# Performance work log

Measured on AMD Instinct MI355X. Metric: run time of the kernel, lower is better.

The kernel has to match this reference:

```python
import jax, jax.numpy as jnp
import numpy as np

N, E, D = 10000, 160000, 256
EPS = 1e-5


def layer_norm(x, gamma, beta):
    mu = jnp.mean(x, axis=-1, keepdims=True)
    var = jnp.var(x, axis=-1, keepdims=True)
    return (x - mu) * jax.lax.rsqrt(var + EPS) * gamma + beta


def mlp(x, w1, b1, w2, b2):
    return jax.nn.relu(x @ w1 + b1) @ w2 + b2


def setup_inputs() -> dict:
    key = jax.random.key(0)
    ks = jax.random.split(key, 16)
    s = lambda fan_in: 1.0 / np.sqrt(fan_in)
    inp = {
        'x': jax.random.normal(ks[0], (N, D), jnp.float32),
        'edge_index': jax.random.randint(ks[1], (2, E), 0, N, jnp.int64),
        'edge_attr': jax.random.normal(ks[2], (E, D), jnp.float32),
        # edge MLP: in 3D=768 -> hidden 2D=512 -> out D=256, then LN
        'e_w1': jax.random.uniform(ks[3], (3 * D, 2 * D), jnp.float32, -s(3 * D), s(3 * D)),
        'e_b1': jnp.zeros((2 * D,), jnp.float32),
        'e_w2': jax.random.uniform(ks[4], (2 * D, D), jnp.float32, -s(2 * D), s(2 * D)),
        'e_b2': jnp.zeros((D,), jnp.float32),
        'e_g': jnp.ones((D,), jnp.float32),
        'e_beta': jnp.zeros((D,), jnp.float32),
        # node MLP: in 2D=512 -> hidden 2D=512 -> out D=256, then LN
        'n_w1': jax.random.uniform(ks[5], (2 * D, 2 * D), jnp.float32, -s(2 * D), s(2 * D)),
        'n_b1': jnp.zeros((2 * D,), jnp.float32),
        'n_w2': jax.random.uniform(ks[6], (2 * D, D), jnp.float32, -s(2 * D), s(2 * D)),
        'n_b2': jnp.zeros((D,), jnp.float32),
        'n_g': jnp.ones((D,), jnp.float32),
        'n_beta': jnp.zeros((D,), jnp.float32),
    }
    return inp


def reference(x, edge_index, edge_attr, e_w1, e_b1, e_w2, e_b2, e_g, e_beta,
              n_w1, n_b1, n_w2, n_b2, n_g, n_beta):
    i, j = edge_index[0], edge_index[1]
    # Edge processor: gather, concat, MLP + LN, residual
    h = jnp.concatenate([x[i], x[j], edge_attr], axis=-1)  # [E, 3D]
    new_edge = edge_attr + layer_norm(mlp(h, e_w1, e_b1, e_w2, e_b2), e_g, e_beta)
    # Node processor: scatter-add over j, concat, MLP + LN, residual
    agg = jax.ops.segment_sum(new_edge, j, num_segments=x.shape[0])  # [N, D]
    hn = jnp.concatenate([x, agg], axis=-1)  # [N, 2D]
    new_x = x + layer_norm(mlp(hn, n_w1, n_b1, n_w2, n_b2), n_g, n_beta)
    return new_x, new_edge
```

## Files before the change

### kernel.cpp

```cpp
#include <hip/hip_runtime.h>

#define NNODE 10000
#define NEDGE 160000
#define DD 256

using f32x4  = __attribute__((ext_vector_type(4))) float;
using bf16x8 = __attribute__((ext_vector_type(8))) short;
using u32x4  = __attribute__((ext_vector_type(4))) unsigned;

__device__ inline short f2bf(float f) {
  unsigned u = __float_as_uint(f);
  unsigned r = (u + 0x7fffu + ((u >> 16) & 1u)) >> 16;
  return (short)(unsigned short)r;
}

__device__ inline float bf2f(short s) {
  return __uint_as_float(((unsigned)(unsigned short)s) << 16);
}

__device__ inline unsigned pkbf(float a, float b) {
  unsigned r;
  asm("v_cvt_pk_bf16_f32 %0, %1, %2" : "=v"(r) : "v"(a), "v"(b));
  return r;
}

__global__ void cast_x_kernel(const float* __restrict__ x, short* __restrict__ xb, int total) {
  int i = blockIdx.x * 256 + threadIdx.x;
  if (i < total) xb[i] = f2bf(x[i]);
}

__global__ void pack_w_kernel(const float* __restrict__ w, short* __restrict__ p, int K, int N) {
  int idx = blockIdx.x * 256 + threadIdx.x;
  if (idx >= K * N) return;
  int k = idx / N, n = idx - k * N;
  p[(size_t)(k >> 3) * N * 8 + (size_t)n * 8 + (k & 7)] = f2bf(w[idx]);
}

__global__ void pack_ew1_kernel(const float* __restrict__ w, short* __restrict__ w1abp,
                                short* __restrict__ w1cp) {
  int idx = blockIdx.x * 256 + threadIdx.x;
  if (idx >= 768 * 512) return;
  int k = idx >> 9, n = idx & 511;
  short v = f2bf(w[idx]);
  if (k < 256) {
    w1abp[(size_t)(k >> 3) * 1024 * 8 + (size_t)n * 8 + (k & 7)] = v;
  } else if (k < 512) {
    int kk = k - 256;
    w1abp[(size_t)(kk >> 3) * 1024 * 8 + (size_t)(512 + n) * 8 + (kk & 7)] = v;
  } else {
    int kk = k - 512;
    w1cp[(size_t)(kk >> 3) * 512 * 8 + (size_t)n * 8 + (kk & 7)] = v;
  }
}

__global__ void hist_kernel(const int* __restrict__ ei, int* __restrict__ deg) {
  int e = blockIdx.x * 256 + threadIdx.x;
  if (e < NEDGE) {
    int j = ei[NEDGE + e]; j = min(max(j, 0), NNODE - 1);
    atomicAdd(&deg[j], 1);
  }
}

__global__ void scan_kernel(const int* __restrict__ deg, int* __restrict__ row_start) {
  __shared__ int part[256];
  int t = threadIdx.x;
  const int CH = 40;
  int base = t * CH;
  int s = 0;
  for (int i = 0; i < CH; i++) {
    int idx = base + i;
    s += (idx < NNODE) ? deg[idx] : 0;
  }
  part[t] = s;
  __syncthreads();
  for (int off = 1; off < 256; off <<= 1) {
    int v = (t >= off) ? part[t - off] : 0;
    __syncthreads();
    part[t] += v;
    __syncthreads();
  }
  int run = (t == 0) ? 0 : part[t - 1];
  for (int i = 0; i < CH; i++) {
    int idx = base + i;
    if (idx < NNODE) { row_start[idx] = run; run += deg[idx]; }
  }
  if (t == 255) row_start[NNODE] = part[255];
}

__global__ void scatter_kernel(const int* __restrict__ ei, const int* __restrict__ row_start,
                               int* __restrict__ cursor, int* __restrict__ csr) {
  int e = blockIdx.x * 256 + threadIdx.x;
  if (e < NEDGE) {
    int j = ei[NEDGE + e]; j = min(max(j, 0), NNODE - 1);
    int p = atomicAdd(&cursor[j], 1);
    csr[row_start[j] + p] = e;
  }
}

__global__ __launch_bounds__(256, 2)
void precomp_pab(const short* __restrict__ xb, const short* __restrict__ w1abp,
                 short* __restrict__ pab) {
  __shared__ __align__(16) short abuf[2048 * 8];

  const int tid  = threadIdx.x;
  const int lane = tid & 63;
  const int wid  = tid >> 6;
  const int lhi  = lane >> 4;
  const int llo  = lane & 15;
  const int swz  = llo & 7;
  const int m0   = blockIdx.x * 64;
  const int h    = blockIdx.y;

  #pragma unroll
  for (int q = 0; q < 8; q++) {
    int S = wid * 512 + q * 64 + lane;
    int row = S >> 5;
    int segp = S & 31;
    int seg = segp ^ (row & 7);
    int rowg = min(m0 + row, NNODE - 1);
    __builtin_amdgcn_global_load_lds(
        (const int*)((const char*)xb + (size_t)rowg * 512 + seg * 16),
        (int*)(abuf + (size_t)(wid * 512 + q * 64) * 8), 16, 0, 0);
  }
  __syncthreads();

  f32x4 acc1[4][8] = {};
  const bf16x8* bp1 = (const bf16x8*)w1abp;
  #pragma unroll
  for (int kk = 0; kk < 256; kk += 32) {
    const int ks = kk >> 3;
    bf16x8 a[4];
    #pragma unroll
    for (int mf = 0; mf < 4; mf++)
      a[mf] = *(const bf16x8*)(abuf + ((mf * 16 + llo) * 32 + ((ks + lhi) ^ swz)) * 8);
    const bf16x8* bb = bp1 + (size_t)(ks + lhi) * 1024 + h * 512 + wid * 128 + llo;
    #pragma unroll
    for (int nf = 0; nf < 8; nf++) {
      bf16x8 b = bb[nf * 16];
      #pragma unroll
      for (int mf = 0; mf < 4; mf++)
        acc1[mf][nf] = __builtin_amdgcn_mfma_f32_16x16x32_bf16(a[mf], b, acc1[mf][nf], 0, 0, 0);
    }
  }

  #pragma unroll
  for (int mf = 0; mf < 4; mf++) {
    #pragma unroll
    for (int r = 0; r < 4; r++) {
      int row = m0 + mf * 16 + lhi * 4 + r;
      if (row < NNODE) {
        u32x4 wv = { pkbf(acc1[mf][0][r], acc1[mf][1][r]),
                     pkbf(acc1[mf][2][r], acc1[mf][3][r]),
                     pkbf(acc1[mf][4][r], acc1[mf][5][r]),
                     pkbf(acc1[mf][6][r], acc1[mf][7][r]) };
        *(u32x4*)(pab + (size_t)row * 1024 + h * 512 + llo * 32 + wid * 8) = wv;
      }
    }
  }
}

__global__ __launch_bounds__(256, 2)
void fused_edge(const int* __restrict__ ei,
                const int* __restrict__ csr,
                const float* __restrict__ ea,
                const short* __restrict__ pab,
                const short* __restrict__ w1cp,
                const float* __restrict__ b1,
                const short* __restrict__ w2p,
                const float* __restrict__ b2,
                const float* __restrict__ gam,
                const float* __restrict__ bet,
                float* __restrict__ out,
                float* __restrict__ aggf)
{
  __shared__ __align__(16) char smem[66560];
  __shared__ int eidx[64], idxi[64], idxj[64];
  __shared__ float pS[256], pQ[256];

  short* abuf = (short*)smem;
  short* hid  = (short*)smem;
  float* outt = (float*)smem;

  const int tid  = threadIdx.x;
  const int lane = tid & 63;
  const int wid  = tid >> 6;
  const int lhi  = lane >> 4;
  const int llo  = lane & 15;
  const int swz  = llo & 7;
  const int m0   = blockIdx.x * 64;
  const int bcol2 = wid * 64 + llo;

  if (tid < 64) {
    int e = csr[m0 + tid];
    eidx[tid] = e;
    int a = ei[e];
    int b = ei[NEDGE + e];
    idxi[tid] = min(max(a, 0), NNODE - 1);
    idxj[tid] = min(max(b, 0), NNODE - 1);
  }
  __syncthreads();

  #pragma unroll
  for (int q = 0; q < 8; q++) {
    int S = q * 256 + tid;
    int row = S >> 5;
    int segp = S & 31;
    int seg = segp ^ (row & 7);
    const f32x4* src = (const f32x4*)(ea + (size_t)eidx[row] * 256 + seg * 8);
    f32x4 u0 = __builtin_nontemporal_load(src);
    f32x4 u1 = __builtin_nontemporal_load(src + 1);
    u32x4 qv = { pkbf(u0.x, u0.y), pkbf(u0.z, u0.w), pkbf(u1.x, u1.y), pkbf(u1.z, u1.w) };
    *(u32x4*)(abuf + (size_t)S * 8) = qv;
  }
  __syncthreads();

  f32x4 acc1[4][8] = {};
  const bf16x8* bp1 = (const bf16x8*)w1cp;
  #pragma unroll
  for (int kk = 0; kk < 256; kk += 32) {
    const int ks = kk >> 3;
    bf16x8 a[4];
    #pragma unroll
    for (int mf = 0; mf < 4; mf++)
      a[mf] = *(const bf16x8*)(abuf + ((mf * 16 + llo) * 32 + ((ks + lhi) ^ swz)) * 8);
    const bf16x8* bb = bp1 + (size_t)(ks + lhi) * 512 + wid * 128 + llo;
    #pragma unroll
    for (int nf = 0; nf < 8; nf++) {
      bf16x8 b = bb[nf * 16];
      #pragma unroll
      for (int mf = 0; mf < 4; mf++)
        acc1[mf][nf] = __builtin_amdgcn_mfma_f32_16x16x32_bf16(a[mf], b, acc1[mf][nf], 0, 0, 0);
    }
  }

  #pragma unroll
  for (int mf = 0; mf < 4; mf++) {
    #pragma unroll
    for (int r = 0; r < 4; r++) {
      int row = mf * 16 + lhi * 4 + r;
      int gi = idxi[row], gj = idxj[row];
      bf16x8 pa = *(const bf16x8*)(pab + (size_t)gi * 1024 + llo * 32 + wid * 8);
      bf16x8 pb = *(const bf16x8*)(pab + (size_t)gj * 1024 + 512 + llo * 32 + wid * 8);
      #pragma unroll
      for (int nf = 0; nf < 8; nf++)
        acc1[mf][nf][r] += bf2f(pa[nf]) + bf2f(pb[nf]);
    }
  }

  float resv[4][4][4];
  #pragma unroll
  for (int mf = 0; mf < 4; mf++) {
    #pragma unroll
    for (int r = 0; r < 4; r++) {
      int row = mf * 16 + lhi * 4 + r;
      #pragma unroll
      for (int nf = 0; nf < 4; nf++) {
        int col = bcol2 + nf * 16;
        resv[mf][r][nf] = bf2f(abuf[row * 256 + (((col >> 3) ^ (row & 7)) << 3) + (col & 7)]);
      }
    }
  }
  __syncthreads();

  #pragma unroll
  for (int nf = 0; nf < 8; nf++) {
    int col = wid * 128 + nf * 16 + llo;
    float bb = b1[col];
    int cs = col >> 3, cl = col & 7;
    #pragma unroll
    for (int mf = 0; mf < 4; mf++) {
      #pragma unroll
      for (int r = 0; r < 4; r++) {
        int row = mf * 16 + lhi * 4 + r;
        float v = acc1[mf][nf][r] + bb;
        v = v > 0.f ? v : 0.f;
        hid[row * 512 + ((cs ^ (row & 7)) * 8) + cl] = f2bf(v);
      }
    }
  }
  __syncthreads();

  f32x4 acc2[4][4] = {};
  const bf16x8* bp2 = (const bf16x8*)w2p;
  #pragma unroll
  for (int kk = 0; kk < 512; kk += 32) {
    const int ks = kk >> 3;
    bf16x8 a[4];
    #pragma unroll
    for (int mf = 0; mf < 4; mf++) {
      int row = mf * 16 + llo;
      a[mf] = *(const bf16x8*)(hid + row * 512 + (((ks + lhi) ^ swz) * 8));
    }
    const bf16x8* bb = bp2 + (size_t)(ks + lhi) * 256 + bcol2;
    #pragma unroll
    for (int nf = 0; nf < 4; nf++) {
      bf16x8 b = bb[nf * 16];
      #pragma unroll
      for (int mf = 0; mf < 4; mf++)
        acc2[mf][nf] = __builtin_amdgcn_mfma_f32_16x16x32_bf16(a[mf], b, acc2[mf][nf], 0, 0, 0);
    }
  }

  float bb2[4], gg[4], be[4];
  #pragma unroll
  for (int nf = 0; nf < 4; nf++) {
    int col = bcol2 + nf * 16;
    bb2[nf] = b2[col]; gg[nf] = gam[col]; be[nf] = bet[col];
  }
  #pragma unroll
  for (int mf = 0; mf < 4; mf++)
    #pragma unroll
    for (int nf = 0; nf < 4; nf++)
      #pragma unroll
      for (int r = 0; r < 4; r++)
        acc2[mf][nf][r] += bb2[nf];

  float S[4][4], Q[4][4];
  #pragma unroll
  for (int mf = 0; mf < 4; mf++) {
    #pragma unroll
    for (int r = 0; r < 4; r++) {
      float s = 0.f, q = 0.f;
      #pragma unroll
      for (int nf = 0; nf < 4; nf++) {
        float v = acc2[mf][nf][r];
        s += v; q += v * v;
      }
      S[mf][r] = s; Q[mf][r] = q;
    }
  }
  #pragma unroll
  for (int m = 1; m <= 8; m <<= 1) {
    #pragma unroll
    for (int mf = 0; mf < 4; mf++)
      #pragma unroll
      for (int r = 0; r < 4; r++) {
        S[mf][r] += __shfl_xor(S[mf][r], m);
        Q[mf][r] += __shfl_xor(Q[mf][r], m);
      }
  }
  if (llo == 0) {
    #pragma unroll
    for (int mf = 0; mf < 4; mf++)
      #pragma unroll
      for (int r = 0; r < 4; r++) {
        int row = mf * 16 + lhi * 4 + r;
        pS[wid * 64 + row] = S[mf][r];
        pQ[wid * 64 + row] = Q[mf][r];
      }
  }
  __syncthreads();

  float mu[4][4], rsv[4][4];
  #pragma unroll
  for (int mf = 0; mf < 4; mf++) {
    #pragma unroll
    for (int r = 0; r < 4; r++) {
      int row = mf * 16 + lhi * 4 + r;
      float s = pS[row] + pS[64 + row] + pS[128 + row] + pS[192 + row];
      float q = pQ[row] + pQ[64 + row] + pQ[128 + row] + pQ[192 + row];
      float m_ = s * (1.f / 256.f);
      mu[mf][r]  = m_;
      rsv[mf][r] = rsqrtf(q * (1.f / 256.f) - m_ * m_ + 1e-5f);
    }
  }

  #pragma unroll
  for (int mf = 0; mf < 4; mf++) {
    #pragma unroll
    for (int r = 0; r < 4; r++) {
      int row = mf * 16 + lhi * 4 + r;
      #pragma unroll
      for (int nf = 0; nf < 4; nf++) {
        float v = (acc2[mf][nf][r] - mu[mf][r]) * rsv[mf][r] * gg[nf] + be[nf]
                  + resv[mf][r][nf];
        outt[row * 260 + bcol2 + nf * 16] = v;
      }
    }
  }
  __syncthreads();

  #pragma unroll
  for (int it = 0; it < 16; it++) {
    int row = it * 4 + wid;
    int e = eidx[row];
    f32x4 o4 = *((const f32x4*)(outt + row * 260) + lane);
    __builtin_nontemporal_store(o4, (f32x4*)(out + (size_t)e * 256) + lane);
  }
  __syncthreads();

  {
    int c = tid;
    float acc = 0.f;
    int cj = idxj[0];
    #pragma unroll 8
    for (int r = 0; r < 64; r++) {
      int jr = idxj[r];
      if (jr != cj) {
        atomicAdd(&aggf[(size_t)cj * 256 + c], acc);
        acc = 0.f; cj = jr;
      }
      acc += outt[r * 260 + c];
    }
    atomicAdd(&aggf[(size_t)cj * 256 + c], acc);
  }
}

__global__ __launch_bounds__(256, 2)
void fused_node(const float* __restrict__ x,
                const short* __restrict__ xb,
                const float* __restrict__ aggf,
                const short* __restrict__ w1p,
                const float* __restrict__ b1,
                const short* __restrict__ w2p,
                const float* __restrict__ b2,
                const float* __restrict__ gam,
                const float* __restrict__ bet,
                float* __restrict__ out)
{
  constexpr int HP = 520;
  __shared__ __align__(16) short hid[64 * HP];
  __shared__ float pS[4][64], pQ[4][64];

  const int tid  = threadIdx.x;
  const int lane = tid & 63;
  const int wid  = tid >> 6;
  const int m0   = blockIdx.x * 64;
  const int lhi  = lane >> 4;
  const int llo  = lane & 15;

  const short* pI[4]; const float* pJ[4];
  #pragma unroll
  for (int mf = 0; mf < 4; mf++) {
    int rr = min(m0 + mf * 16 + llo, NNODE - 1);
    pI[mf] = xb + (size_t)rr * DD;
    pJ[mf] = aggf + (size_t)rr * DD;
  }

  f32x4 acc1[4][8] = {};
  const bf16x8* bp1 = (const bf16x8*)w1p;
  const int bcol1 = wid * 128 + llo;

  #pragma unroll
  for (int s = 0; s < 8; s++) {
    #pragma unroll
    for (int kk = 0; kk < 64; kk += 32) {
      const int ko = s * 64 + kk + lhi * 8;
      bf16x8 a[4];
      #pragma unroll
      for (int mf = 0; mf < 4; mf++) {
        if (s < 4) {
          a[mf] = *(const bf16x8*)(pI[mf] + ko);
        } else {
          const float* fp = pJ[mf] + (ko - 256);
          f32x4 u0 = *(const f32x4*)fp;
          f32x4 u1 = *(const f32x4*)(fp + 4);
          u32x4 q = { pkbf(u0.x, u0.y), pkbf(u0.z, u0.w),
                      pkbf(u1.x, u1.y), pkbf(u1.z, u1.w) };
          a[mf] = __builtin_bit_cast(bf16x8, q);
        }
      }
      const bf16x8* bb = bp1 + (size_t)(s * 8 + (kk >> 3) + lhi) * 512 + bcol1;
      #pragma unroll
      for (int nf = 0; nf < 8; nf++) {
        bf16x8 b = bb[nf * 16];
        #pragma unroll
        for (int mf = 0; mf < 4; mf++)
          acc1[mf][nf] = __builtin_amdgcn_mfma_f32_16x16x32_bf16(a[mf], b, acc1[mf][nf], 0, 0, 0);
      }
    }
  }

  #pragma unroll
  for (int nf = 0; nf < 8; nf++) {
    int col = wid * 128 + nf * 16 + llo;
    float bb = b1[col];
    #pragma unroll
    for (int mf = 0; mf < 4; mf++) {
      #pragma unroll
      for (int r = 0; r < 4; r++) {
        float v = acc1[mf][nf][r] + bb;
        v = v > 0.f ? v : 0.f;
        hid[(mf * 16 + lhi * 4 + r) * HP + col] = f2bf(v);
      }
    }
  }
  __syncthreads();

  f32x4 acc2[4][4] = {};
  const bf16x8* bp2 = (const bf16x8*)w2p;
  const int bcol2 = wid * 64 + llo;
  #pragma unroll
  for (int kk = 0; kk < 512; kk += 32) {
    bf16x8 a[4];
    #pragma unroll
    for (int mf = 0; mf < 4; mf++)
      a[mf] = *(const bf16x8*)(hid + (mf * 16 + llo) * HP + kk + lhi * 8);
    const bf16x8* bb = bp2 + (size_t)((kk >> 3) + lhi) * 256 + bcol2;
    #pragma unroll
    for (int nf = 0; nf < 4; nf++) {
      bf16x8 b = bb[nf * 16];
      #pragma unroll
      for (int mf = 0; mf < 4; mf++)
        acc2[mf][nf] = __builtin_amdgcn_mfma_f32_16x16x32_bf16(a[mf], b, acc2[mf][nf], 0, 0, 0);
    }
  }

  float bb2[4], gg[4], be[4];
  #pragma unroll
  for (int nf = 0; nf < 4; nf++) {
    int col = bcol2 + nf * 16;
    bb2[nf] = b2[col]; gg[nf] = gam[col]; be[nf] = bet[col];
  }
  #pragma unroll
  for (int mf = 0; mf < 4; mf++)
    #pragma unroll
    for (int nf = 0; nf < 4; nf++)
      #pragma unroll
      for (int r = 0; r < 4; r++)
        acc2[mf][nf][r] += bb2[nf];

  float S[4][4], Q[4][4];
  #pragma unroll
  for (int mf = 0; mf < 4; mf++) {
    #pragma unroll
    for (int r = 0; r < 4; r++) {
      float s = 0.f, q = 0.f;
      #pragma unroll
      for (int nf = 0; nf < 4; nf++) {
        float v = acc2[mf][nf][r];
        s += v; q += v * v;
      }
      S[mf][r] = s; Q[mf][r] = q;
    }
  }
  #pragma unroll
  for (int m = 1; m <= 8; m <<= 1) {
    #pragma unroll
    for (int mf = 0; mf < 4; mf++)
      #pragma unroll
      for (int r = 0; r < 4; r++) {
        S[mf][r] += __shfl_xor(S[mf][r], m);
        Q[mf][r] += __shfl_xor(Q[mf][r], m);
      }
  }
  if (llo == 0) {
    #pragma unroll
    for (int mf = 0; mf < 4; mf++)
      #pragma unroll
      for (int r = 0; r < 4; r++) {
        int row = mf * 16 + lhi * 4 + r;
        pS[wid][row] = S[mf][r];
        pQ[wid][row] = Q[mf][r];
      }
  }
  __syncthreads();

  float mu[4][4], rsv[4][4];
  #pragma unroll
  for (int mf = 0; mf < 4; mf++) {
    #pragma unroll
    for (int r = 0; r < 4; r++) {
      int row = mf * 16 + lhi * 4 + r;
      float s = pS[0][row] + pS[1][row] + pS[2][row] + pS[3][row];
      float q = pQ[0][row] + pQ[1][row] + pQ[2][row] + pQ[3][row];
      float m_ = s * (1.f / 256.f);
      mu[mf][r]  = m_;
      rsv[mf][r] = rsqrtf(q * (1.f / 256.f) - m_ * m_ + 1e-5f);
    }
  }

  #pragma unroll
  for (int mf = 0; mf < 4; mf++) {
    #pragma unroll
    for (int r = 0; r < 4; r++) {
      int grow = m0 + mf * 16 + lhi * 4 + r;
      if (grow >= NNODE) continue;
      const float* rp = x   + (size_t)grow * DD + bcol2;
      float*       op = out + (size_t)grow * DD + bcol2;
      #pragma unroll
      for (int nf = 0; nf < 4; nf++) {
        float v = (acc2[mf][nf][r] - mu[mf][r]) * rsv[mf][r] * gg[nf] + be[nf] + rp[nf * 16];
        op[nf * 16] = v;
      }
    }
  }
}

extern "C" void kernel_launch(void* const* d_in, const int* in_sizes, int n_in,
                              void* d_out, int out_size, void* d_ws, size_t ws_size,
                              hipStream_t stream) {
  const float* x      = (const float*)d_in[0];
  const int*   ei     = (const int*)  d_in[1];
  const float* ea     = (const float*)d_in[2];
  const float* e_w1   = (const float*)d_in[3];
  const float* e_b1   = (const float*)d_in[4];
  const float* e_w2   = (const float*)d_in[5];
  const float* e_b2   = (const float*)d_in[6];
  const float* e_g    = (const float*)d_in[7];
  const float* e_beta = (const float*)d_in[8];
  const float* n_w1   = (const float*)d_in[9];
  const float* n_b1   = (const float*)d_in[10];
  const float* n_w2   = (const float*)d_in[11];
  const float* n_b2   = (const float*)d_in[12];
  const float* n_g    = (const float*)d_in[13];
  const float* n_beta = (const float*)d_in[14];

  float* out_x = (float*)d_out;
  float* out_e = (float*)d_out + (size_t)NNODE * DD;

  char* w = (char*)d_ws;
  short* xb    = (short*)(w);
  short* pab   = (short*)(w + 5120000);
  short* w1abp = (short*)(w + 25600000);
  short* w1cp  = (short*)(w + 26124288);
  short* ew2p  = (short*)(w + 26386432);
  short* nw1p  = (short*)(w + 26648576);
  short* nw2p  = (short*)(w + 27172864);
  float* aggf  = (float*)(w + 27435008);
  int*   deg   = (int*)  (w + 37675008);
  int*   cur   = (int*)  (w + 37715968);
  int*   rs    = (int*)  (w + 37756928);
  int*   csr   = (int*)  (w + 37797904);

  hipMemsetAsync(deg, 0, 81920, stream);
  hipMemsetAsync(aggf, 0, (size_t)NNODE * DD * sizeof(float), stream);

  cast_x_kernel<<<(NNODE * DD + 255) / 256, 256, 0, stream>>>(x, xb, NNODE * DD);
  pack_ew1_kernel<<<(768 * 512 + 255) / 256, 256, 0, stream>>>(e_w1, w1abp, w1cp);
  pack_w_kernel<<<(512 * 512 + 255) / 256, 256, 0, stream>>>(n_w1, nw1p, 512, 512);
  pack_w_kernel<<<(512 * 256 + 255) / 256, 256, 0, stream>>>(e_w2, ew2p, 512, 256);
  pack_w_kernel<<<(512 * 256 + 255) / 256, 256, 0, stream>>>(n_w2, nw2p, 512, 256);

  hist_kernel<<<(NEDGE + 255) / 256, 256, 0, stream>>>(ei, deg);
  scan_kernel<<<1, 256, 0, stream>>>(deg, rs);
  scatter_kernel<<<(NEDGE + 255) / 256, 256, 0, stream>>>(ei, rs, cur, csr);

  precomp_pab<<<dim3((NNODE + 63) / 64, 2), 256, 0, stream>>>(xb, w1abp, pab);

  fused_edge<<<NEDGE / 64, 256, 0, stream>>>(ei, csr, ea, pab, w1cp, e_b1,
                                             ew2p, e_b2, e_g, e_beta, out_e, aggf);
  fused_node<<<(NNODE + 63) / 64, 256, 0, stream>>>(x, xb, aggf, nw1p, n_b1,
                                                    nw2p, n_b2, n_g, n_beta, out_x);
}
```

Baseline: 452.1 us.

## Compute x[i] projection in edge kernel instead of precomputing per node

The x[i]·W1a term is now computed per edge inside fused_edge. Each block gathers the bf16 rows of x for source nodes into LDS and runs an extra 256-deep MFMA pass. Only the x[j]·W1b term is still precomputed per node, which halves precomp_pab and the pab buffer. This trades a random bf16 gather of precomputed rows for more matrix work per edge and more LDS use. The CSR sort by j keeps the j gathers local, but the i gathers are scattered either way.

```diff
diff --git a/kernel.cpp b/kernel.cpp
--- a/kernel.cpp
+++ b/kernel.cpp
@@ -36,21 +36,15 @@
   p[(size_t)(k >> 3) * N * 8 + (size_t)n * 8 + (k & 7)] = f2bf(w[idx]);
 }
 
-__global__ void pack_ew1_kernel(const float* __restrict__ w, short* __restrict__ w1abp,
-                                short* __restrict__ w1cp) {
+__global__ void pack_ew1_kernel(const float* __restrict__ w, short* __restrict__ w1ap,
+                                short* __restrict__ w1bp, short* __restrict__ w1cp) {
   int idx = blockIdx.x * 256 + threadIdx.x;
   if (idx >= 768 * 512) return;
   int k = idx >> 9, n = idx & 511;
   short v = f2bf(w[idx]);
-  if (k < 256) {
-    w1abp[(size_t)(k >> 3) * 1024 * 8 + (size_t)n * 8 + (k & 7)] = v;
-  } else if (k < 512) {
-    int kk = k - 256;
-    w1abp[(size_t)(kk >> 3) * 1024 * 8 + (size_t)(512 + n) * 8 + (kk & 7)] = v;
-  } else {
-    int kk = k - 512;
-    w1cp[(size_t)(kk >> 3) * 512 * 8 + (size_t)n * 8 + (kk & 7)] = v;
-  }
+  int kk = k & 255;
+  short* dst = (k < 256) ? w1ap : (k < 512) ? w1bp : w1cp;
+  dst[(size_t)(kk >> 3) * 512 * 8 + (size_t)n * 8 + (kk & 7)] = v;
 }
 
 __global__ void hist_kernel(const int* __restrict__ ei, int* __restrict__ deg) {
@@ -98,7 +92,7 @@
 }
 
 __global__ __launch_bounds__(256, 2)
-void precomp_pab(const short* __restrict__ xb, const short* __restrict__ w1abp,
+void precomp_pab(const short* __restrict__ xb, const short* __restrict__ w1bp,
                  short* __restrict__ pab) {
   __shared__ __align__(16) short abuf[2048 * 8];
 
@@ -109,7 +103,6 @@
   const int llo  = lane & 15;
   const int swz  = llo & 7;
   const int m0   = blockIdx.x * 64;
-  const int h    = blockIdx.y;
 
   #pragma unroll
   for (int q = 0; q < 8; q++) {
@@ -125,7 +118,7 @@
   __syncthreads();
 
   f32x4 acc1[4][8] = {};
-  const bf16x8* bp1 = (const bf16x8*)w1abp;
+  const bf16x8* bp1 = (const bf16x8*)w1bp;
   #pragma unroll
   for (int kk = 0; kk < 256; kk += 32) {
     const int ks = kk >> 3;
@@ -133,7 +126,7 @@
     #pragma unroll
     for (int mf = 0; mf < 4; mf++)
       a[mf] = *(const bf16x8*)(abuf + ((mf * 16 + llo) * 32 + ((ks + lhi) ^ swz)) * 8);
-    const bf16x8* bb = bp1 + (size_t)(ks + lhi) * 1024 + h * 512 + wid * 128 + llo;
+    const bf16x8* bb = bp1 + (size_t)(ks + lhi) * 512 + wid * 128 + llo;
     #pragma unroll
     for (int nf = 0; nf < 8; nf++) {
       bf16x8 b = bb[nf * 16];
@@ -153,7 +146,7 @@
                      pkbf(acc1[mf][2][r], acc1[mf][3][r]),
                      pkbf(acc1[mf][4][r], acc1[mf][5][r]),
                      pkbf(acc1[mf][6][r], acc1[mf][7][r]) };
-        *(u32x4*)(pab + (size_t)row * 1024 + h * 512 + llo * 32 + wid * 8) = wv;
+        *(u32x4*)(pab + (size_t)row * 512 + llo * 32 + wid * 8) = wv;
       }
     }
   }
@@ -163,7 +156,9 @@
 void fused_edge(const int* __restrict__ ei,
                 const int* __restrict__ csr,
                 const float* __restrict__ ea,
+                const short* __restrict__ xb,
                 const short* __restrict__ pab,
+                const short* __restrict__ w1ap,
                 const short* __restrict__ w1cp,
                 const float* __restrict__ b1,
                 const short* __restrict__ w2p,
@@ -177,9 +172,10 @@
   __shared__ int eidx[64], idxi[64], idxj[64];
   __shared__ float pS[256], pQ[256];
 
-  short* abuf = (short*)smem;
-  short* hid  = (short*)smem;
-  float* outt = (float*)smem;
+  short* abufE = (short*)smem;
+  short* abufX = (short*)(smem + 32768);
+  short* hid   = (short*)smem;
+  float* outt  = (float*)smem;
 
   const int tid  = threadIdx.x;
   const int lane = tid & 63;
@@ -199,6 +195,17 @@
     idxj[tid] = min(max(b, 0), NNODE - 1);
   }
   __syncthreads();
+
+  #pragma unroll
+  for (int q = 0; q < 8; q++) {
+    int S = wid * 512 + q * 64 + lane;
+    int row = S >> 5;
+    int segp = S & 31;
+    int seg = segp ^ (row & 7);
+    __builtin_amdgcn_global_load_lds(
+        (const int*)((const char*)xb + (size_t)idxi[row] * 512 + seg * 16),
+        (int*)(abufX + (size_t)(wid * 512 + q * 64) * 8), 16, 0, 0);
+  }
 
   #pragma unroll
   for (int q = 0; q < 8; q++) {
@@ -210,26 +217,45 @@
     f32x4 u0 = __builtin_nontemporal_load(src);
     f32x4 u1 = __builtin_nontemporal_load(src + 1);
     u32x4 qv = { pkbf(u0.x, u0.y), pkbf(u0.z, u0.w), pkbf(u1.x, u1.y), pkbf(u1.z, u1.w) };
-    *(u32x4*)(abuf + (size_t)S * 8) = qv;
+    *(u32x4*)(abufE + (size_t)S * 8) = qv;
   }
   __syncthreads();
 
   f32x4 acc1[4][8] = {};
-  const bf16x8* bp1 = (const bf16x8*)w1cp;
-  #pragma unroll
-  for (int kk = 0; kk < 256; kk += 32) {
-    const int ks = kk >> 3;
-    bf16x8 a[4];
-    #pragma unroll
-    for (int mf = 0; mf < 4; mf++)
-      a[mf] = *(const bf16x8*)(abuf + ((mf * 16 + llo) * 32 + ((ks + lhi) ^ swz)) * 8);
-    const bf16x8* bb = bp1 + (size_t)(ks + lhi) * 512 + wid * 128 + llo;
-    #pragma unroll
-    for (int nf = 0; nf < 8; nf++) {
-      bf16x8 b = bb[nf * 16];
+  {
+    const bf16x8* bpC = (const bf16x8*)w1cp;
+    #pragma unroll
+    for (int kk = 0; kk < 256; kk += 32) {
+      const int ks = kk >> 3;
+      bf16x8 a[4];
       #pragma unroll
       for (int mf = 0; mf < 4; mf++)
-        acc1[mf][nf] = __builtin_amdgcn_mfma_f32_16x16x32_bf16(a[mf], b, acc1[mf][nf], 0, 0, 0);
+        a[mf] = *(const bf16x8*)(abufE + ((mf * 16 + llo) * 32 + ((ks + lhi) ^ swz)) * 8);
+      const bf16x8* bb = bpC + (size_t)(ks + lhi) * 512 + wid * 128 + llo;
+      #pragma unroll
+      for (int nf = 0; nf < 8; nf++) {
+        bf16x8 b = bb[nf * 16];
+        #pragma unroll
+        for (int mf = 0; mf < 4; mf++)
+          acc1[mf][nf] = __builtin_amdgcn_mfma_f32_16x16x32_bf16(a[mf], b, acc1[mf][nf], 0, 0, 0);
+      }
+    }
+    const bf16x8* bpA = (const bf16x8*)w1ap;
+    #pragma unroll
+    for (int kk = 0; kk < 256; kk += 32) {
+      const int ks = kk >> 3;
+      bf16x8 a[4];
+      #pragma unroll
+      for (int mf = 0; mf < 4; mf++)
+        a[mf] = *(const bf16x8*)(abufX + ((mf * 16 + llo) * 32 + ((ks + lhi) ^ swz)) * 8);
+      const bf16x8* bb = bpA + (size_t)(ks + lhi) * 512 + wid * 128 + llo;
+      #pragma unroll
+      for (int nf = 0; nf < 8; nf++) {
+        bf16x8 b = bb[nf * 16];
+        #pragma unroll
+        for (int mf = 0; mf < 4; mf++)
+          acc1[mf][nf] = __builtin_amdgcn_mfma_f32_16x16x32_bf16(a[mf], b, acc1[mf][nf], 0, 0, 0);
+      }
     }
   }
 
@@ -238,12 +264,11 @@
     #pragma unroll
     for (int r = 0; r < 4; r++) {
       int row = mf * 16 + lhi * 4 + r;
-      int gi = idxi[row], gj = idxj[row];
-      bf16x8 pa = *(const bf16x8*)(pab + (size_t)gi * 1024 + llo * 32 + wid * 8);
-      bf16x8 pb = *(const bf16x8*)(pab + (size_t)gj * 1024 + 512 + llo * 32 + wid * 8);
+      int gj = idxj[row];
+      bf16x8 pb = *(const bf16x8*)(pab + (size_t)gj * 512 + llo * 32 + wid * 8);
       #pragma unroll
       for (int nf = 0; nf < 8; nf++)
-        acc1[mf][nf][r] += bf2f(pa[nf]) + bf2f(pb[nf]);
+        acc1[mf][nf][r] += bf2f(pb[nf]);
     }
   }
 
@@ -256,7 +281,7 @@
       #pragma unroll
       for (int nf = 0; nf < 4; nf++) {
         int col = bcol2 + nf * 16;
-        resv[mf][r][nf] = bf2f(abuf[row * 256 + (((col >> 3) ^ (row & 7)) << 3) + (col & 7)]);
+        resv[mf][r][nf] = bf2f(abufE[row * 256 + (((col >> 3) ^ (row & 7)) << 3) + (col & 7)]);
       }
     }
   }
@@ -612,22 +637,23 @@
   char* w = (char*)d_ws;
   short* xb    = (short*)(w);
   short* pab   = (short*)(w + 5120000);
-  short* w1abp = (short*)(w + 25600000);
-  short* w1cp  = (short*)(w + 26124288);
-  short* ew2p  = (short*)(w + 26386432);
-  short* nw1p  = (short*)(w + 26648576);
-  short* nw2p  = (short*)(w + 27172864);
-  float* aggf  = (float*)(w + 27435008);
-  int*   deg   = (int*)  (w + 37675008);
-  int*   cur   = (int*)  (w + 37715968);
-  int*   rs    = (int*)  (w + 37756928);
-  int*   csr   = (int*)  (w + 37797904);
+  short* w1ap  = (short*)(w + 15360000);
+  short* w1bp  = (short*)(w + 15622144);
+  short* w1cp  = (short*)(w + 15884288);
+  short* ew2p  = (short*)(w + 16146432);
+  short* nw1p  = (short*)(w + 16408576);
+  short* nw2p  = (short*)(w + 16932864);
+  float* aggf  = (float*)(w + 17195008);
+  int*   deg   = (int*)  (w + 27435008);
+  int*   cur   = (int*)  (w + 27475968);
+  int*   rs    = (int*)  (w + 27516928);
+  int*   csr   = (int*)  (w + 27557904);
 
   hipMemsetAsync(deg, 0, 81920, stream);
   hipMemsetAsync(aggf, 0, (size_t)NNODE * DD * sizeof(float), stream);
 
   cast_x_kernel<<<(NNODE * DD + 255) / 256, 256, 0, stream>>>(x, xb, NNODE * DD);
-  pack_ew1_kernel<<<(768 * 512 + 255) / 256, 256, 0, stream>>>(e_w1, w1abp, w1cp);
+  pack_ew1_kernel<<<(768 * 512 + 255) / 256, 256, 0, stream>>>(e_w1, w1ap, w1bp, w1cp);
   pack_w_kernel<<<(512 * 512 + 255) / 256, 256, 0, stream>>>(n_w1, nw1p, 512, 512);
   pack_w_kernel<<<(512 * 256 + 255) / 256, 256, 0, stream>>>(e_w2, ew2p, 512, 256);
   pack_w_kernel<<<(512 * 256 + 255) / 256, 256, 0, stream>>>(n_w2, nw2p, 512, 256);
@@ -636,9 +662,9 @@
   scan_kernel<<<1, 256, 0, stream>>>(deg, rs);
   scatter_kernel<<<(NEDGE + 255) / 256, 256, 0, stream>>>(ei, rs, cur, csr);
 
-  precomp_pab<<<dim3((NNODE + 63) / 64, 2), 256, 0, stream>>>(xb, w1abp, pab);
-
-  fused_edge<<<NEDGE / 64, 256, 0, stream>>>(ei, csr, ea, pab, w1cp, e_b1,
+  precomp_pab<<<(NNODE + 63) / 64, 256, 0, stream>>>(xb, w1bp, pab);
+
+  fused_edge<<<NEDGE / 64, 256, 0, stream>>>(ei, csr, ea, xb, pab, w1ap, w1cp, e_b1,
                                              ew2p, e_b2, e_g, e_beta, out_e, aggf);
   fused_node<<<(NNODE + 63) / 64, 256, 0, stream>>>(x, xb, aggf, nw1p, n_b1,
                                                     nw2p, n_b2, n_g, n_beta, out_x);
```

New measurement: 541.5 us. +19.8%, slower.
